# Kernel tuning notes

Measured on AMD Instinct MI355X. Metric: run time of the kernel, lower is better.

The kernel has to match this reference:

```python
import jax, jax.numpy as jnp
import numpy as np

# Faithful JAX version of ROIMask_To_Img / paste_mask_in_image (Mask R-CNN paste):
# per box: (mask+1)/2, zero-pad by 1, expand box by (M+2)/M, truncate to int,
# bilinear-resize (align_corners=False, edge-clamped) to the box extent, and
# overwrite-paste into the image canvas; final canvas is mapped to [-1, 1].
# Instead of per-box dynamic-size interpolate + slice assignment, we evaluate the
# bilinear resample densely over the full image grid and mask to the box region
# (same math, jit-compatible, single fused gather-resize-scatter).


def _edge_coords(s, size):
    # torch bilinear align_corners=False with edge clamping
    s = jnp.clip(s, 0.0, size - 1.0)
    i0 = jnp.floor(s)
    t = s - i0
    i0 = i0.astype(jnp.int32)
    i1 = jnp.minimum(i0 + 1, size - 1)
    return i0, i1, t


def _paste_step(im, mask, box):
    # im: [H, W] canvas; mask: [M, M] in [-1,1]; box: [4] float (x0, y0, x1, y1)
    H, W = im.shape
    M = mask.shape[-1]
    Mp = M + 2  # padded mask size
    m = jnp.pad((mask + 1.0) * 0.5, 1)  # expand_masks(padding=1) -> [Mp, Mp]
    scale = (M + 2.0) / M
    w_half = (box[2] - box[0]) * (0.5 * scale)
    h_half = (box[3] - box[1]) * (0.5 * scale)
    x_c = (box[2] + box[0]) * 0.5
    y_c = (box[3] + box[1]) * 0.5
    # expand_boxes then .to(int32) (truncation toward zero, like torch)
    b = jnp.trunc(jnp.stack([x_c - w_half, y_c - h_half,
                             x_c + w_half, y_c + h_half])).astype(jnp.int32)
    w = jnp.maximum(b[2] - b[0] + 1, 1).astype(jnp.float32)
    h = jnp.maximum(b[3] - b[1] + 1, 1).astype(jnp.float32)
    px = jnp.arange(H)
    py = jnp.arange(W)
    # source coords in padded-mask space (align_corners=False)
    sx = (px - b[0] + 0.5) * (Mp / w) - 0.5  # [H]
    sy = (py - b[1] + 0.5) * (Mp / h) - 0.5  # [W]
    x0, x1, tx = _edge_coords(sx, Mp)
    y0, y1, ty = _edge_coords(sy, Mp)
    # separable bilinear: mix rows first ([H, Mp]), then columns ([H, W])
    rowmix = m[x0] * (1.0 - tx)[:, None] + m[x1] * tx[:, None]
    val = rowmix[:, y0] * (1.0 - ty)[None, :] + rowmix[:, y1] * ty[None, :]
    # paste region (overwrite semantics, clipped to the image)
    vx = (px >= b[0]) & (px <= b[2])
    vy = (py >= b[1]) & (py <= b[3])
    return jnp.where(vx[:, None] & vy[None, :], val, im)


def setup_inputs() -> dict:
    key = jax.random.key(0)
    B, N, M, H, W = 32, 16, 28, 1024, 1024
    k1, k2, k3, k4 = jax.random.split(key, 4)
    masks = jax.random.uniform(k1, (B, N, 1, M, M), jnp.float32, -1.0, 1.0)
    # valid boxes inside the image: corner + extent
    p0 = jax.random.uniform(k2, (B, N, 2), jnp.float32, 0.0, H - 64.0)
    ext = jax.random.uniform(k3, (B, N, 2), jnp.float32, 16.0, 200.0)
    p1 = jnp.minimum(p0 + ext, H - 2.0)
    rects = jnp.concatenate([p0, p1], axis=-1)  # [B, N, 4] = (x0, y0, x1, y1)
    instance_mask = jnp.zeros((B, 1, H, W), jnp.float32)
    return {"masks": masks, "rects": rects, "instance_mask": instance_mask}


def reference(masks, rects, instance_mask):
    # masks: [B, N, 1, M, M]; rects: [B, N, 4]; instance_mask: [B, 1, H, W]
    H, W = instance_mask.shape[-2], instance_mask.shape[-1]

    def per_image(masks_b, rects_b):
        im0 = jnp.zeros((H, W), jnp.float32)
        def step(im, xs):
            m, bx = xs
            return _paste_step(im, m, bx), None
        im, _ = jax.lax.scan(step, im0, (masks_b[:, 0], rects_b))
        return im

    im = jax.vmap(per_image)(masks, rects)  # [B, H, W]
    return im[:, None, :, :] * 2.0 - 1.0
```

## Files before the change

### kernel.cpp

```cpp
#include <hip/hip_runtime.h>

constexpr int Bc  = 32;
constexpr int Nc  = 16;
constexpr int Mc  = 28;
constexpr int MPc = 30;
constexpr int Hc  = 1024;
constexpr int Wc  = 1024;
constexpr int ROWS = 8;

__global__ __launch_bounds__(256)
void paste_masks_kernel(const float* __restrict__ masks,
                        const float* __restrict__ rects,
                        float* __restrict__ out)
{
    const int tiles_per_img = Hc / ROWS;
    const int bid  = blockIdx.x;
    const int b    = bid / tiles_per_img;
    const int row0 = (bid - b * tiles_per_img) * ROWS;
    const int tid  = threadIdx.x;

    __shared__ int      s_r0[Nc], s_r2[Nc];
    __shared__ int      s_c1[Nc], s_c3[Nc];
    __shared__ float    s_sxs[Nc], s_sys[Nc];
    __shared__ unsigned s_rowmask[ROWS];

    if (tid < Nc) {
        const float* r = rects + (b * Nc + tid) * 4;
        const float x0 = r[0], y0 = r[1], x1 = r[2], y1 = r[3];
        const float hs = 0.5357142857142857f;
        const float w_half = (x1 - x0) * hs;
        const float h_half = (y1 - y0) * hs;
        const float xc = (x1 + x0) * 0.5f;
        const float yc = (y1 + y0) * 0.5f;
        const int ib0 = (int)truncf(xc - w_half);
        const int ib1 = (int)truncf(yc - h_half);
        const int ib2 = (int)truncf(xc + w_half);
        const int ib3 = (int)truncf(yc + h_half);
        s_r0[tid] = ib0; s_r2[tid] = ib2;
        s_c1[tid] = ib1; s_c3[tid] = ib3;
        const float w = fmaxf((float)(ib2 - ib0 + 1), 1.0f);
        const float h = fmaxf((float)(ib3 - ib1 + 1), 1.0f);
        s_sxs[tid] = (float)MPc / w;
        s_sys[tid] = (float)MPc / h;
    }
    __syncthreads();

    if (tid < ROWS) {
        const int row = row0 + tid;
        unsigned m = 0;
        #pragma unroll
        for (int n = 0; n < Nc; ++n)
            if (row >= s_r0[n] && row <= s_r2[n]) m |= (1u << n);
        s_rowmask[tid] = m;
    }

    const int col0 = tid * 4;
    unsigned cmask[4];
    #pragma unroll
    for (int c = 0; c < 4; ++c) {
        const int col = col0 + c;
        unsigned m = 0;
        #pragma unroll
        for (int n = 0; n < Nc; ++n)
            if (col >= s_c1[n] && col <= s_c3[n]) m |= (1u << n);
        cmask[c] = m;
    }
    __syncthreads();

    const float* mbase = masks + (size_t)b * (Nc * Mc * Mc);
    float* orow = out + (size_t)b * Hc * Wc + (size_t)row0 * Wc;

    for (int rr = 0; rr < ROWS; ++rr) {
        const int row = row0 + rr;
        const unsigned rm = s_rowmask[rr];
        float4 v;
        float* vp = (float*)&v;
        #pragma unroll
        for (int c = 0; c < 4; ++c) {
            const unsigned m = cmask[c] & rm;
            float val = -1.0f;
            if (m) {
                const int n = 31 - __clz((int)m);
                float sx = ((float)(row - s_r0[n]) + 0.5f) * s_sxs[n] - 0.5f;
                sx = fminf(fmaxf(sx, 0.0f), (float)(MPc - 1));
                const int   i0 = (int)floorf(sx);
                const float tx = sx - (float)i0;
                const int   i1 = min(i0 + 1, MPc - 1);

                const int col = col0 + c;
                float sy = ((float)(col - s_c1[n]) + 0.5f) * s_sys[n] - 0.5f;
                sy = fminf(fmaxf(sy, 0.0f), (float)(MPc - 1));
                const int   j0 = (int)floorf(sy);
                const float ty = sy - (float)j0;
                const int   j1 = min(j0 + 1, MPc - 1);

                const float* mp = mbase + n * (Mc * Mc);
                const bool iok0 = (i0 >= 1) & (i0 <= Mc);
                const bool iok1 = (i1 >= 1) & (i1 <= Mc);
                const bool jok0 = (j0 >= 1) & (j0 <= Mc);
                const bool jok1 = (j1 >= 1) & (j1 <= Mc);
                const float m00 = (iok0 & jok0) ? (mp[(i0-1)*Mc + (j0-1)] + 1.0f) * 0.5f : 0.0f;
                const float m10 = (iok1 & jok0) ? (mp[(i1-1)*Mc + (j0-1)] + 1.0f) * 0.5f : 0.0f;
                const float m01 = (iok0 & jok1) ? (mp[(i0-1)*Mc + (j1-1)] + 1.0f) * 0.5f : 0.0f;
                const float m11 = (iok1 & jok1) ? (mp[(i1-1)*Mc + (j1-1)] + 1.0f) * 0.5f : 0.0f;
                const float a0 = m00 * (1.0f - tx) + m10 * tx;
                const float a1 = m01 * (1.0f - tx) + m11 * tx;
                val = (a0 * (1.0f - ty) + a1 * ty) * 2.0f - 1.0f;
            }
            vp[c] = val;
        }
        *((float4*)(orow + (size_t)rr * Wc) + tid) = v;
    }
}

extern "C" void kernel_launch(void* const* d_in, const int* in_sizes, int n_in,
                              void* d_out, int out_size, void* d_ws, size_t ws_size,
                              hipStream_t stream) {
    const float* masks = (const float*)d_in[0];
    const float* rects = (const float*)d_in[1];
    float* out = (float*)d_out;

    const int grid = Bc * (Hc / ROWS);
    paste_masks_kernel<<<grid, 256, 0, stream>>>(masks, rects, out);
}
```

Baseline: 250.7 us.

## Split into background fill kernel and per-box scatter paste kernel

```diff
diff --git a/kernel.cpp b/kernel.cpp
--- a/kernel.cpp
+++ b/kernel.cpp
@@ -6,111 +6,103 @@
 constexpr int MPc = 30;
 constexpr int Hc  = 1024;
 constexpr int Wc  = 1024;
-constexpr int ROWS = 8;
+constexpr int NBOX = Bc * Nc;
+constexpr int MAXROWS = 224;
+
 
 __global__ __launch_bounds__(256)
-void paste_masks_kernel(const float* __restrict__ masks,
-                        const float* __restrict__ rects,
+void fill_and_prep_kernel(const float* __restrict__ rects,
+                          float4* __restrict__ out, int n4,
+                          int4* __restrict__ rectbuf,
+                          float2* __restrict__ scalebuf)
+{
+    if (blockIdx.x == 0) {
+        #pragma unroll
+        for (int i = 0; i < 2; ++i) {
+            const int box = threadIdx.x + i * 256;
+            const float* r = rects + box * 4;
+            const float x0 = r[0], y0 = r[1], x1 = r[2], y1 = r[3];
+            const float hs = 0.5357142857142857f;
+            const float w_half = (x1 - x0) * hs;
+            const float h_half = (y1 - y0) * hs;
+            const float xc = (x1 + x0) * 0.5f;
+            const float yc = (y1 + y0) * 0.5f;
+            const int ib0 = (int)truncf(xc - w_half);
+            const int ib1 = (int)truncf(yc - h_half);
+            const int ib2 = (int)truncf(xc + w_half);
+            const int ib3 = (int)truncf(yc + h_half);
+            rectbuf[box] = make_int4(ib0, ib1, ib2, ib3);
+            const float w = fmaxf((float)(ib2 - ib0 + 1), 1.0f);
+            const float h = fmaxf((float)(ib3 - ib1 + 1), 1.0f);
+            scalebuf[box] = make_float2((float)MPc / w, (float)MPc / h);
+        }
+    }
+    const float4 v = make_float4(-1.0f, -1.0f, -1.0f, -1.0f);
+    const int stride = gridDim.x * 256;
+    for (int i = blockIdx.x * 256 + threadIdx.x; i < n4; i += stride)
+        out[i] = v;
+}
+
+__global__ __launch_bounds__(256)
+void paste_boxes_kernel(const float* __restrict__ masks,
+                        const int4* __restrict__ rectbuf,
+                        const float2* __restrict__ scalebuf,
                         float* __restrict__ out)
 {
-    const int tiles_per_img = Hc / ROWS;
-    const int bid  = blockIdx.x;
-    const int b    = bid / tiles_per_img;
-    const int row0 = (bid - b * tiles_per_img) * ROWS;
-    const int tid  = threadIdx.x;
+    const int box = blockIdx.x;
+    const int b   = box >> 4;
+    const int n   = box & (Nc - 1);
 
-    __shared__ int      s_r0[Nc], s_r2[Nc];
-    __shared__ int      s_c1[Nc], s_c3[Nc];
-    __shared__ float    s_sxs[Nc], s_sys[Nc];
-    __shared__ unsigned s_rowmask[ROWS];
+    const int4 rc = rectbuf[box];
+    const int rlo = max(rc.x, 0);
+    const int rhi = min(rc.z, Hc - 1);
+    const int row = rlo + (int)blockIdx.y;
+    if (row > rhi) return;
 
-    if (tid < Nc) {
-        const float* r = rects + (b * Nc + tid) * 4;
-        const float x0 = r[0], y0 = r[1], x1 = r[2], y1 = r[3];
-        const float hs = 0.5357142857142857f;
-        const float w_half = (x1 - x0) * hs;
-        const float h_half = (y1 - y0) * hs;
-        const float xc = (x1 + x0) * 0.5f;
-        const float yc = (y1 + y0) * 0.5f;
-        const int ib0 = (int)truncf(xc - w_half);
-        const int ib1 = (int)truncf(yc - h_half);
-        const int ib2 = (int)truncf(xc + w_half);
-        const int ib3 = (int)truncf(yc + h_half);
-        s_r0[tid] = ib0; s_r2[tid] = ib2;
-        s_c1[tid] = ib1; s_c3[tid] = ib3;
-        const float w = fmaxf((float)(ib2 - ib0 + 1), 1.0f);
-        const float h = fmaxf((float)(ib3 - ib1 + 1), 1.0f);
-        s_sxs[tid] = (float)MPc / w;
-        s_sys[tid] = (float)MPc / h;
+    const int clo = max(rc.y, 0);
+    const int chi = min(rc.w, Wc - 1);
+    if (clo + (int)(threadIdx.x & 0xFFFFFFC0u) > chi) return;
+    const int col = clo + (int)threadIdx.x;
+
+    bool covered = false;
+    #pragma unroll
+    for (int k = 0; k < Nc; ++k) {
+        if (k > n) {
+            const int4 kc = rectbuf[b * Nc + k];
+            if (row >= kc.x && row <= kc.z)
+                covered |= (col >= kc.y && col <= kc.w);
+        }
     }
-    __syncthreads();
+    if (col > chi || covered) return;
 
-    if (tid < ROWS) {
-        const int row = row0 + tid;
-        unsigned m = 0;
-        #pragma unroll
-        for (int n = 0; n < Nc; ++n)
-            if (row >= s_r0[n] && row <= s_r2[n]) m |= (1u << n);
-        s_rowmask[tid] = m;
-    }
+    const float2 sc = scalebuf[box];
 
-    const int col0 = tid * 4;
-    unsigned cmask[4];
-    #pragma unroll
-    for (int c = 0; c < 4; ++c) {
-        const int col = col0 + c;
-        unsigned m = 0;
-        #pragma unroll
-        for (int n = 0; n < Nc; ++n)
-            if (col >= s_c1[n] && col <= s_c3[n]) m |= (1u << n);
-        cmask[c] = m;
-    }
-    __syncthreads();
+    float sx = ((float)(row - rc.x) + 0.5f) * sc.x - 0.5f;
+    sx = fminf(fmaxf(sx, 0.0f), (float)(MPc - 1));
+    const int   i0 = (int)floorf(sx);
+    const float tx = sx - (float)i0;
+    const int   i1 = min(i0 + 1, MPc - 1);
 
-    const float* mbase = masks + (size_t)b * (Nc * Mc * Mc);
-    float* orow = out + (size_t)b * Hc * Wc + (size_t)row0 * Wc;
+    float sy = ((float)(col - rc.y) + 0.5f) * sc.y - 0.5f;
+    sy = fminf(fmaxf(sy, 0.0f), (float)(MPc - 1));
+    const int   j0 = (int)floorf(sy);
+    const float ty = sy - (float)j0;
+    const int   j1 = min(j0 + 1, MPc - 1);
 
-    for (int rr = 0; rr < ROWS; ++rr) {
-        const int row = row0 + rr;
-        const unsigned rm = s_rowmask[rr];
-        float4 v;
-        float* vp = (float*)&v;
-        #pragma unroll
-        for (int c = 0; c < 4; ++c) {
-            const unsigned m = cmask[c] & rm;
-            float val = -1.0f;
-            if (m) {
-                const int n = 31 - __clz((int)m);
-                float sx = ((float)(row - s_r0[n]) + 0.5f) * s_sxs[n] - 0.5f;
-                sx = fminf(fmaxf(sx, 0.0f), (float)(MPc - 1));
-                const int   i0 = (int)floorf(sx);
-                const float tx = sx - (float)i0;
-                const int   i1 = min(i0 + 1, MPc - 1);
+    const float* mp = masks + (size_t)box * (Mc * Mc);
+    const bool iok0 = (i0 >= 1) & (i0 <= Mc);
+    const bool iok1 = (i1 >= 1) & (i1 <= Mc);
+    const bool jok0 = (j0 >= 1) & (j0 <= Mc);
+    const bool jok1 = (j1 >= 1) & (j1 <= Mc);
+    const float m00 = (iok0 & jok0) ? (mp[(i0-1)*Mc + (j0-1)] + 1.0f) * 0.5f : 0.0f;
+    const float m10 = (iok1 & jok0) ? (mp[(i1-1)*Mc + (j0-1)] + 1.0f) * 0.5f : 0.0f;
+    const float m01 = (iok0 & jok1) ? (mp[(i0-1)*Mc + (j1-1)] + 1.0f) * 0.5f : 0.0f;
+    const float m11 = (iok1 & jok1) ? (mp[(i1-1)*Mc + (j1-1)] + 1.0f) * 0.5f : 0.0f;
+    const float a0 = m00 * (1.0f - tx) + m10 * tx;
+    const float a1 = m01 * (1.0f - tx) + m11 * tx;
+    const float val = (a0 * (1.0f - ty) + a1 * ty) * 2.0f - 1.0f;
 
-                const int col = col0 + c;
-                float sy = ((float)(col - s_c1[n]) + 0.5f) * s_sys[n] - 0.5f;
-                sy = fminf(fmaxf(sy, 0.0f), (float)(MPc - 1));
-                const int   j0 = (int)floorf(sy);
-                const float ty = sy - (float)j0;
-                const int   j1 = min(j0 + 1, MPc - 1);
-
-                const float* mp = mbase + n * (Mc * Mc);
-                const bool iok0 = (i0 >= 1) & (i0 <= Mc);
-                const bool iok1 = (i1 >= 1) & (i1 <= Mc);
-                const bool jok0 = (j0 >= 1) & (j0 <= Mc);
-                const bool jok1 = (j1 >= 1) & (j1 <= Mc);
-                const float m00 = (iok0 & jok0) ? (mp[(i0-1)*Mc + (j0-1)] + 1.0f) * 0.5f : 0.0f;
-                const float m10 = (iok1 & jok0) ? (mp[(i1-1)*Mc + (j0-1)] + 1.0f) * 0.5f : 0.0f;
-                const float m01 = (iok0 & jok1) ? (mp[(i0-1)*Mc + (j1-1)] + 1.0f) * 0.5f : 0.0f;
-                const float m11 = (iok1 & jok1) ? (mp[(i1-1)*Mc + (j1-1)] + 1.0f) * 0.5f : 0.0f;
-                const float a0 = m00 * (1.0f - tx) + m10 * tx;
-                const float a1 = m01 * (1.0f - tx) + m11 * tx;
-                val = (a0 * (1.0f - ty) + a1 * ty) * 2.0f - 1.0f;
-            }
-            vp[c] = val;
-        }
-        *((float4*)(orow + (size_t)rr * Wc) + tid) = v;
-    }
+    out[(size_t)b * Hc * Wc + (size_t)row * Wc + col] = val;
 }
 
 extern "C" void kernel_launch(void* const* d_in, const int* in_sizes, int n_in,
@@ -120,6 +112,12 @@
     const float* rects = (const float*)d_in[1];
     float* out = (float*)d_out;
 
-    const int grid = Bc * (Hc / ROWS);
-    paste_masks_kernel<<<grid, 256, 0, stream>>>(masks, rects, out);
+    int4*   rectbuf  = (int4*)d_ws;
+    float2* scalebuf = (float2*)((char*)d_ws + 8192);
+
+    fill_and_prep_kernel<<<2048, 256, 0, stream>>>(rects, (float4*)out,
+                                                   out_size / 4, rectbuf, scalebuf);
+
+    dim3 grid2(NBOX, MAXROWS);
+    paste_boxes_kernel<<<grid2, 256, 0, stream>>>(masks, rectbuf, scalebuf, out);
 }
```

Result: slower. 296.8 us (+18.4%).
